# Optimization experiments

Measured on AMD Instinct MI355X. Metric: run time of the kernel, lower is better.

Reference implementation:

```python
import jax, jax.numpy as jnp
import numpy as np

K = 3          # kernel size
KF = K * K     # kernel field = 9
PAD = 1
STRIDE = 1


def _conv(x, w, b):
    y = jax.lax.conv_general_dilated(
        x, w, (STRIDE, STRIDE), [(PAD, PAD), (PAD, PAD)],
        dimension_numbers=('NCHW', 'OIHW', 'NCHW'))
    return y + b[None, :, None, None]


def _bilinear_gather(x, py, px):
    # x: [B,C,H,W]; py/px: [B,KF,Ho,Wo] float sampling coords (zero-pad outside)
    B, C, H, W = x.shape
    xf = x.reshape(B, C, H * W)
    y0 = jnp.floor(py)
    x0 = jnp.floor(px)

    def corner(yc, xc):
        wy = 1.0 - jnp.abs(py - yc)
        wx = 1.0 - jnp.abs(px - xc)
        valid = (yc >= 0) & (yc <= H - 1) & (xc >= 0) & (xc <= W - 1)
        yi = jnp.clip(yc, 0, H - 1).astype(jnp.int32)
        xi = jnp.clip(xc, 0, W - 1).astype(jnp.int32)
        idx = (yi * W + xi).reshape(B, -1)               # [B, KF*Ho*Wo]
        v = jax.vmap(lambda f, i: f[:, i])(xf, idx)      # [B, C, KF*Ho*Wo]
        wgt = (wy * wx * valid.astype(x.dtype)).reshape(B, 1, -1)
        return v * wgt

    return (corner(y0, x0) + corner(y0, x0 + 1) +
            corner(y0 + 1, x0) + corner(y0 + 1, x0 + 1))  # [B,C,KF*Ho*Wo]


def _deform_conv(x, offset, mask, w, b):
    # modulated deformable conv v2 (mmcv offset layout: [y,x] interleaved per kernel pt)
    B, C, H, W = x.shape
    Ho, Wo = mask.shape[2], mask.shape[3]
    kh, kw = jnp.meshgrid(jnp.arange(K), jnp.arange(K), indexing='ij')
    kh = kh.reshape(-1).astype(x.dtype)   # [KF]
    kw = kw.reshape(-1).astype(x.dtype)
    base_y = (jnp.arange(Ho) * STRIDE - PAD).astype(x.dtype)
    base_x = (jnp.arange(Wo) * STRIDE - PAD).astype(x.dtype)
    off = offset.reshape(B, KF, 2, Ho, Wo)
    py = base_y[None, None, :, None] + kh[None, :, None, None] + off[:, :, 0]
    px = base_x[None, None, None, :] + kw[None, :, None, None] + off[:, :, 1]
    val = _bilinear_gather(x, py, px).reshape(B, C, KF, Ho, Wo)
    val = val * mask[:, None]                             # modulate
    out = jnp.einsum('bckhw,ock->bohw', val, w.reshape(w.shape[0], C, KF))
    return out + b[None, :, None, None]


def setup_inputs() -> dict:
    key = jax.random.key(0)
    k1, k2, k3 = jax.random.split(key, 3)
    B, C, H, W = 8, 64, 128, 128
    x = jax.random.normal(k1, (B, C, H, W), dtype=jnp.float32)
    w_om = jax.random.normal(k2, (3 * KF, C, K, K), dtype=jnp.float32) * 0.02
    b_om = jnp.zeros((3 * KF,), dtype=jnp.float32)
    w_dc = jax.random.normal(k3, (64, C, K, K), dtype=jnp.float32) * 0.05
    b_dc = jnp.zeros((64,), dtype=jnp.float32)
    return {"x": x, "w_om": w_om, "b_om": b_om, "w_dc": w_dc, "b_dc": b_dc}


def reference(x, w_om, b_om, w_dc, b_dc):
    om = _conv(x, w_om, b_om)                 # [B, 3*KF, H, W]
    offset = om[:, :2 * KF]
    mask = 2.0 * jax.nn.sigmoid(om[:, 2 * KF:])
    return _deform_conv(x, offset, mask, w_dc, b_dc)
```

## Files before the change

### kernel.cpp

```cpp
#include <hip/hip_runtime.h>
#include <cmath>

#define IH 128
#define IW 128
#define NB 8

typedef __attribute__((ext_vector_type(8))) short bf16x8;
typedef __attribute__((ext_vector_type(4))) float f32x4;

union U4B8 { uint4 u; bf16x8 h; };

#define OFFM_OFF 0
#define XT_OFF   3538944
#define WTDC_OFF (3538944 + 4194304)
#define WTOM_OFF (3538944 + 4194304 + 18432)

__device__ __forceinline__ unsigned short f32_to_bf16(float f) {
    unsigned int u = __float_as_uint(f);
    u += 0x7fffu + ((u >> 16) & 1u);
    return (unsigned short)(u >> 16);
}

__global__ void transpose_weights(const float* __restrict__ w_dc,
                                  const float* __restrict__ w_om,
                                  unsigned short* __restrict__ wt_dc16,
                                  unsigned short* __restrict__ wt_om16) {
    int idx = blockIdx.x * blockDim.x + threadIdx.x;
    if (idx < 9 * 64 * 64) {
        int k = idx >> 12;
        int o = (idx >> 6) & 63;
        int c = idx & 63;
        wt_dc16[idx] = f32_to_bf16(w_dc[(o * 64 + c) * 9 + k]);
    }
    if (idx < 9 * 32 * 64) {
        int k = idx >> 11;
        int o = (idx >> 6) & 31;
        int c = idx & 63;
        wt_om16[idx] = (o < 27) ? f32_to_bf16(w_om[(o * 64 + c) * 9 + k])
                                : (unsigned short)0;
    }
}

__global__ __launch_bounds__(256) void transpose_x(
        const float* __restrict__ x, unsigned short* __restrict__ xT) {
    __shared__ float t[64 * 65];
    const int tid = threadIdx.x;
    const int blk = blockIdx.x;
    const int b = blk >> 8;
    const int rem = blk & 255;
    const int h = rem >> 1;
    const int w0 = (rem & 1) << 6;

    for (int i = tid; i < 4096; i += 256) {
        const int c = i >> 6;
        const int w = i & 63;
        t[w * 65 + c] = x[(((size_t)(b * 64 + c)) << 14) + (h << 7) + w0 + w];
    }
    __syncthreads();
    const int c2 = (tid & 31) * 2;
    ushort2* dst = (ushort2*)(xT + (((size_t)b << 20)) + ((size_t)((h << 7) + w0)) * 64 + c2);
#pragma unroll
    for (int p = 0; p < 8; ++p) {
        const int w = (tid >> 5) + p * 8;
        ushort2 u;
        u.x = f32_to_bf16(t[w * 65 + c2]);
        u.y = f32_to_bf16(t[w * 65 + c2 + 1]);
        dst[(size_t)w * 32] = u;
    }
}

__global__ __launch_bounds__(256) void conv_om_mfma(
        const unsigned short* __restrict__ xT,
        const float* __restrict__ b_om,
        const unsigned short* __restrict__ wt_om16,
        float* __restrict__ offm) {
    __shared__ __align__(16) unsigned short win[198 * 72];
    __shared__ __align__(16) unsigned short wks[2][32 * 72];

    const int tid = threadIdx.x;
    const int bid = blockIdx.x;
    const int swz = ((bid & 7) << 8) + (bid >> 3);
    const int b = swz >> 8;
    const int rem = swz & 255;
    const int h = rem >> 1;
    const int w0 = (rem & 1) << 6;
    const int wid = tid >> 6;
    const int lane = tid & 63;
    const int ln15 = lane & 15;
    const int quad = lane >> 4;

    for (int idx = tid; idx < 1584; idx += 256) {
        const int pos = idx >> 3;
        const int part = idx & 7;
        const int r = pos / 66;
        const int xx = pos - r * 66;
        const int y = h + r - 1;
        const int xg = w0 + xx - 1;
        uint4 v = make_uint4(0u, 0u, 0u, 0u);
        if (y >= 0 && y < IH && xg >= 0 && xg < IW)
            v = *(const uint4*)(xT + (((size_t)b << 20) + (((y << 7) + xg) << 6) + (part << 3)));
        *(uint4*)&win[pos * 72 + part * 8] = v;
    }
    {
        const int o = tid >> 3;
        const int part = tid & 7;
        *(uint4*)&wks[0][o * 72 + part * 8] =
            *(const uint4*)(wt_om16 + (o << 6) + (part << 3));
    }
    __syncthreads();

    f32x4 acc[2] = {{0.f, 0.f, 0.f, 0.f}, {0.f, 0.f, 0.f, 0.f}};

    for (int k = 0; k < 9; ++k) {
        const int buf = k & 1;
        if (k < 8) {
            const int o = tid >> 3;
            const int part = tid & 7;
            *(uint4*)&wks[buf ^ 1][o * 72 + part * 8] =
                *(const uint4*)(wt_om16 + ((k + 1) << 11) + (o << 6) + (part << 3));
        }
        const int kh = k / 3;
        const int kw = k - kh * 3;
        const int posb = kh * 66 + wid * 16 + ln15 + kw;
        const unsigned short* wb = wks[buf];
#pragma unroll
        for (int ch = 0; ch < 2; ++ch) {
            const int c = (ch << 5) + (quad << 3);
            U4B8 a, b0, b1;
            a.u  = *(const uint4*)&win[posb * 72 + c];
            b0.u = *(const uint4*)&wb[ln15 * 72 + c];
            b1.u = *(const uint4*)&wb[(16 + ln15) * 72 + c];
            acc[0] = __builtin_amdgcn_mfma_f32_16x16x32_bf16(a.h, b0.h, acc[0], 0, 0, 0);
            acc[1] = __builtin_amdgcn_mfma_f32_16x16x32_bf16(a.h, b1.h, acc[1], 0, 0, 0);
        }
        __syncthreads();
    }

    const int px0 = wid * 16 + quad * 4;
#pragma unroll
    for (int ot = 0; ot < 2; ++ot) {
        const int o = (ot << 4) + ln15;
        if (o >= 27) continue;
        const float bias = b_om[o];
        float4 r;
        r.x = acc[ot][0] + bias;
        r.y = acc[ot][1] + bias;
        r.z = acc[ot][2] + bias;
        r.w = acc[ot][3] + bias;
        if (o >= 18) {
            r.x = 2.0f / (1.0f + __expf(-r.x));
            r.y = 2.0f / (1.0f + __expf(-r.y));
            r.z = 2.0f / (1.0f + __expf(-r.z));
            r.w = 2.0f / (1.0f + __expf(-r.w));
        }
        *(float4*)&offm[(((size_t)(b * 27 + o)) << 14) + (h << 7) + w0 + px0] = r;
    }
}

__device__ __forceinline__ void corner2(const unsigned short* __restrict__ p,
                                        float wgt, float* v) {
    const uint4 a = *(const uint4*)p;
    const uint4 c = *(const uint4*)(p + 32);
    unsigned int u[8] = {a.x, a.y, a.z, a.w, c.x, c.y, c.z, c.w};
#pragma unroll
    for (int i = 0; i < 8; ++i) {
        v[2 * i]     += wgt * __uint_as_float(u[i] << 16);
        v[2 * i + 1] += wgt * __uint_as_float(u[i] & 0xffff0000u);
    }
}

__device__ __forceinline__ void gather_frags(
        const unsigned short* __restrict__ xb, const float* __restrict__ offs,
        int k, int lpx, int h, int w0, int quad, U4B8& a0, U4B8& a1) {
    const float offy = offs[(k << 1) * 64 + lpx];
    const float offx = offs[((k << 1) + 1) * 64 + lpx];
    const float msk  = offs[(18 + k) * 64 + lpx];
    const int kh = k / 3;
    const int kw = k - kh * 3;
    const float py  = (float)(h + kh - 1) + offy;
    const float pxf = (float)(w0 + lpx + kw - 1) + offx;
    const float y0f = floorf(py);
    const float x0f = floorf(pxf);
    const float fy = py - y0f;
    const float fx = pxf - x0f;
    const float wy0 = 1.0f - fy, wx0 = 1.0f - fx;
    const float vy0 = (y0f >= 0.0f && y0f <= 127.0f) ? 1.0f : 0.0f;
    const float vy1 = (y0f >= -1.0f && y0f <= 126.0f) ? 1.0f : 0.0f;
    const float vx0 = (x0f >= 0.0f && x0f <= 127.0f) ? 1.0f : 0.0f;
    const float vx1 = (x0f >= -1.0f && x0f <= 126.0f) ? 1.0f : 0.0f;
    const float w00 = wy0 * wx0 * vy0 * vx0;
    const float w01 = wy0 * fx  * vy0 * vx1;
    const float w10 = fy  * wx0 * vy1 * vx0;
    const float w11 = fy  * fx  * vy1 * vx1;
    const int y0i = min(max((int)y0f, 0), 127);
    const int y1i = min(max((int)y0f + 1, 0), 127);
    const int x0i = min(max((int)x0f, 0), 127);
    const int x1i = min(max((int)x0f + 1, 0), 127);

    float v[16];
#pragma unroll
    for (int i = 0; i < 16; ++i) v[i] = 0.0f;
    const int cofs = quad << 3;
    corner2(xb + ((((size_t)((y0i << 7) + x0i)) << 6) + cofs), w00, v);
    corner2(xb + ((((size_t)((y0i << 7) + x1i)) << 6) + cofs), w01, v);
    corner2(xb + ((((size_t)((y1i << 7) + x0i)) << 6) + cofs), w10, v);
    corner2(xb + ((((size_t)((y1i << 7) + x1i)) << 6) + cofs), w11, v);

    unsigned int pk[8];
#pragma unroll
    for (int i = 0; i < 8; ++i) {
        const unsigned int lo = f32_to_bf16(v[2 * i] * msk);
        const unsigned int hi = f32_to_bf16(v[2 * i + 1] * msk);
        pk[i] = lo | (hi << 16);
    }
    a0.u = make_uint4(pk[0], pk[1], pk[2], pk[3]);
    a1.u = make_uint4(pk[4], pk[5], pk[6], pk[7]);
}

__global__ __launch_bounds__(256) void deform_mfma(
        const unsigned short* __restrict__ xT,
        const float* __restrict__ b_dc,
        const float* __restrict__ offm,
        const unsigned short* __restrict__ wt_dc16,
        float* __restrict__ out) {
    __shared__ __align__(16) float offs[27 * 64];
    __shared__ __align__(16) unsigned short wks[2][64 * 72];

    const int tid = threadIdx.x;
    const int bid = blockIdx.x;
    const int swz = ((bid & 7) << 8) + (bid >> 3);
    const int b = swz >> 8;
    const int rem = swz & 255;
    const int h = rem >> 1;
    const int w0 = (rem & 1) << 6;
    const int wid = tid >> 6;
    const int lane = tid & 63;
    const int ln15 = lane & 15;
    const int quad = lane >> 4;
    const int lpx = (wid << 4) + ln15;

    for (int i = tid; i < 1728; i += 256) {
        const int ch = i >> 6;
        const int px = i & 63;
        offs[i] = offm[(((size_t)(b * 27 + ch)) << 14) + (h << 7) + w0 + px];
    }
    for (int s = tid; s < 512; s += 256) {
        const int o = s >> 3;
        const int part = s & 7;
        *(uint4*)&wks[0][o * 72 + part * 8] =
            *(const uint4*)(wt_dc16 + (o << 6) + (part << 3));
    }
    __syncthreads();

    const unsigned short* xb = xT + ((size_t)b << 20);

    f32x4 acc[4];
#pragma unroll
    for (int i = 0; i < 4; ++i) acc[i] = (f32x4){0.f, 0.f, 0.f, 0.f};

    U4B8 a0c, a1c;
    gather_frags(xb, offs, 0, lpx, h, w0, quad, a0c, a1c);

    for (int k = 0; k < 9; ++k) {
        const int buf = k & 1;
        U4B8 a0n, a1n;
        a0n.u = make_uint4(0u, 0u, 0u, 0u);
        a1n.u = make_uint4(0u, 0u, 0u, 0u);
        if (k < 8) {
            for (int s = tid; s < 512; s += 256) {
                const int o = s >> 3;
                const int part = s & 7;
                *(uint4*)&wks[buf ^ 1][o * 72 + part * 8] =
                    *(const uint4*)(wt_dc16 + ((k + 1) << 12) + (o << 6) + (part << 3));
            }
            gather_frags(xb, offs, k + 1, lpx, h, w0, quad, a0n, a1n);
        }
        const unsigned short* wb = wks[buf];
#pragma unroll
        for (int ot = 0; ot < 4; ++ot) {
            U4B8 b0, b1;
            const unsigned short* base = &wb[((ot << 4) + ln15) * 72 + (quad << 3)];
            b0.u = *(const uint4*)base;
            b1.u = *(const uint4*)(base + 32);
            acc[ot] = __builtin_amdgcn_mfma_f32_16x16x32_bf16(a0c.h, b0.h, acc[ot], 0, 0, 0);
            acc[ot] = __builtin_amdgcn_mfma_f32_16x16x32_bf16(a1c.h, b1.h, acc[ot], 0, 0, 0);
        }
        __syncthreads();
        a0c = a0n;
        a1c = a1n;
    }

#pragma unroll
    for (int ot = 0; ot < 4; ++ot) {
        const int o = (ot << 4) + ln15;
        const float bias = b_dc[o];
        float4 r;
        r.x = acc[ot][0] + bias;
        r.y = acc[ot][1] + bias;
        r.z = acc[ot][2] + bias;
        r.w = acc[ot][3] + bias;
        *(float4*)&out[(((size_t)(b * 64 + o)) << 14) + (h << 7) + w0 + (wid << 4) + (quad << 2)] = r;
    }
}

extern "C" void kernel_launch(void* const* d_in, const int* in_sizes, int n_in,
                              void* d_out, int out_size, void* d_ws, size_t ws_size,
                              hipStream_t stream) {
    const float* x    = (const float*)d_in[0];
    const float* w_om = (const float*)d_in[1];
    const float* b_om = (const float*)d_in[2];
    const float* w_dc = (const float*)d_in[3];
    const float* b_dc = (const float*)d_in[4];
    float* out = (float*)d_out;
    float* ws  = (float*)d_ws;

    float* offm = ws + OFFM_OFF;
    unsigned short* xT      = (unsigned short*)(ws + XT_OFF);
    unsigned short* wt_dc16 = (unsigned short*)(ws + WTDC_OFF);
    unsigned short* wt_om16 = (unsigned short*)(ws + WTOM_OFF);

    const int n_blocks = NB * IH * (IW / 64);

    transpose_weights<<<144, 256, 0, stream>>>(w_dc, w_om, wt_dc16, wt_om16);
    transpose_x<<<NB * IH * 2, 256, 0, stream>>>(x, xT);
    conv_om_mfma<<<n_blocks, 256, 0, stream>>>(xT, b_om, wt_om16, offm);
    deform_mfma<<<n_blocks, 256, 0, stream>>>(xT, b_dc, offm, wt_dc16, out);
}
```

Baseline: 182.8 us.

## Split bilinear gather into async issue and deferred packed-FMA combine

The deformable gather is split in two. Raw corner loads for the next kernel point are issued a full iteration ahead and held in registers, and the bilinear combine runs just before the MFMAs. The combine now uses v_pk_fma_f32 with the mask folded into the corner weights, plus v_cvt_pk_bf16_f32 for packing. The weight tile prefetch goes through registers, the k-loop is fully unrolled, and the trailing barrier is replaced with a raw s_barrier after an lgkmcnt wait. This aims to hide gather latency behind the MFMA work and cut VALU instructions, at the cost of more registers (16 uint4 live) and a lighter synchronisation that depends on the manual waitcnt being correct.

Result: faster. 177.6 us (-2.9%).

```diff
diff --git a/kernel.cpp b/kernel.cpp
--- a/kernel.cpp
+++ b/kernel.cpp
@@ -7,6 +7,7 @@
 
 typedef __attribute__((ext_vector_type(8))) short bf16x8;
 typedef __attribute__((ext_vector_type(4))) float f32x4;
+typedef __attribute__((ext_vector_type(2))) float f32x2;
 
 union U4B8 { uint4 u; bf16x8 h; };
 
@@ -157,21 +158,9 @@
     }
 }
 
-__device__ __forceinline__ void corner2(const unsigned short* __restrict__ p,
-                                        float wgt, float* v) {
-    const uint4 a = *(const uint4*)p;
-    const uint4 c = *(const uint4*)(p + 32);
-    unsigned int u[8] = {a.x, a.y, a.z, a.w, c.x, c.y, c.z, c.w};
-#pragma unroll
-    for (int i = 0; i < 8; ++i) {
-        v[2 * i]     += wgt * __uint_as_float(u[i] << 16);
-        v[2 * i + 1] += wgt * __uint_as_float(u[i] & 0xffff0000u);
-    }
-}
-
-__device__ __forceinline__ void gather_frags(
+__device__ __forceinline__ void issue_gather(
         const unsigned short* __restrict__ xb, const float* __restrict__ offs,
-        int k, int lpx, int h, int w0, int quad, U4B8& a0, U4B8& a1) {
+        int k, int lpx, int h, int w0, int quad, uint4* g, float* cw) {
     const float offy = offs[(k << 1) * 64 + lpx];
     const float offx = offs[((k << 1) + 1) * 64 + lpx];
     const float msk  = offs[(18 + k) * 64 + lpx];
@@ -188,31 +177,51 @@
     const float vy1 = (y0f >= -1.0f && y0f <= 126.0f) ? 1.0f : 0.0f;
     const float vx0 = (x0f >= 0.0f && x0f <= 127.0f) ? 1.0f : 0.0f;
     const float vx1 = (x0f >= -1.0f && x0f <= 126.0f) ? 1.0f : 0.0f;
-    const float w00 = wy0 * wx0 * vy0 * vx0;
-    const float w01 = wy0 * fx  * vy0 * vx1;
-    const float w10 = fy  * wx0 * vy1 * vx0;
-    const float w11 = fy  * fx  * vy1 * vx1;
+    cw[0] = wy0 * wx0 * vy0 * vx0 * msk;
+    cw[1] = wy0 * fx  * vy0 * vx1 * msk;
+    cw[2] = fy  * wx0 * vy1 * vx0 * msk;
+    cw[3] = fy  * fx  * vy1 * vx1 * msk;
     const int y0i = min(max((int)y0f, 0), 127);
     const int y1i = min(max((int)y0f + 1, 0), 127);
     const int x0i = min(max((int)x0f, 0), 127);
     const int x1i = min(max((int)x0f + 1, 0), 127);
-
-    float v[16];
-#pragma unroll
-    for (int i = 0; i < 16; ++i) v[i] = 0.0f;
     const int cofs = quad << 3;
-    corner2(xb + ((((size_t)((y0i << 7) + x0i)) << 6) + cofs), w00, v);
-    corner2(xb + ((((size_t)((y0i << 7) + x1i)) << 6) + cofs), w01, v);
-    corner2(xb + ((((size_t)((y1i << 7) + x0i)) << 6) + cofs), w10, v);
-    corner2(xb + ((((size_t)((y1i << 7) + x1i)) << 6) + cofs), w11, v);
-
+    const unsigned short* p00 = xb + ((((size_t)((y0i << 7) + x0i)) << 6) + cofs);
+    const unsigned short* p01 = xb + ((((size_t)((y0i << 7) + x1i)) << 6) + cofs);
+    const unsigned short* p10 = xb + ((((size_t)((y1i << 7) + x0i)) << 6) + cofs);
+    const unsigned short* p11 = xb + ((((size_t)((y1i << 7) + x1i)) << 6) + cofs);
+    g[0] = *(const uint4*)p00;  g[1] = *(const uint4*)(p00 + 32);
+    g[2] = *(const uint4*)p01;  g[3] = *(const uint4*)(p01 + 32);
+    g[4] = *(const uint4*)p10;  g[5] = *(const uint4*)(p10 + 32);
+    g[6] = *(const uint4*)p11;  g[7] = *(const uint4*)(p11 + 32);
+}
+
+__device__ __forceinline__ void pack_frags(const uint4* g, const float* cw,
+                                           U4B8& a0, U4B8& a1) {
+    f32x2 v2[8];
+#pragma unroll
+    for (int i = 0; i < 8; ++i) v2[i] = (f32x2){0.f, 0.f};
+#pragma unroll
+    for (int c = 0; c < 4; ++c) {
+        f32x2 w2;
+        w2.x = cw[c];
+        w2.y = cw[c];
+        const uint4 ga = g[2 * c];
+        const uint4 gb = g[2 * c + 1];
+        const unsigned int u[8] = {ga.x, ga.y, ga.z, ga.w, gb.x, gb.y, gb.z, gb.w};
+#pragma unroll
+        for (int i = 0; i < 8; ++i) {
+            f32x2 x2;
+            x2.x = __uint_as_float(u[i] << 16);
+            x2.y = __uint_as_float(u[i] & 0xffff0000u);
+            asm("v_pk_fma_f32 %0, %1, %2, %0" : "+v"(v2[i]) : "v"(x2), "v"(w2));
+        }
+    }
     unsigned int pk[8];
 #pragma unroll
-    for (int i = 0; i < 8; ++i) {
-        const unsigned int lo = f32_to_bf16(v[2 * i] * msk);
-        const unsigned int hi = f32_to_bf16(v[2 * i + 1] * msk);
-        pk[i] = lo | (hi << 16);
-    }
+    for (int i = 0; i < 8; ++i)
+        asm("v_cvt_pk_bf16_f32 %0, %1, %2"
+            : "=v"(pk[i]) : "v"(v2[i].x), "v"(v2[i].y));
     a0.u = make_uint4(pk[0], pk[1], pk[2], pk[3]);
     a1.u = make_uint4(pk[4], pk[5], pk[6], pk[7]);
 }
@@ -239,17 +248,14 @@
     const int quad = lane >> 4;
     const int lpx = (wid << 4) + ln15;
 
+    const int so0 = tid >> 3, sp0 = tid & 7;
+    const int so1 = (tid + 256) >> 3, sp1 = tid & 7;
+
     for (int i = tid; i < 1728; i += 256) {
-        const int ch = i >> 6;
-        const int px = i & 63;
-        offs[i] = offm[(((size_t)(b * 27 + ch)) << 14) + (h << 7) + w0 + px];
-    }
-    for (int s = tid; s < 512; s += 256) {
-        const int o = s >> 3;
-        const int part = s & 7;
-        *(uint4*)&wks[0][o * 72 + part * 8] =
-            *(const uint4*)(wt_dc16 + (o << 6) + (part << 3));
-    }
+        offs[i] = offm[(((size_t)(b * 27 + (i >> 6))) << 14) + (h << 7) + w0 + (i & 63)];
+    }
+    *(uint4*)&wks[0][so0 * 72 + sp0 * 8] = *(const uint4*)(wt_dc16 + (so0 << 6) + (sp0 << 3));
+    *(uint4*)&wks[0][so1 * 72 + sp1 * 8] = *(const uint4*)(wt_dc16 + (so1 << 6) + (sp1 << 3));
     __syncthreads();
 
     const unsigned short* xb = xT + ((size_t)b << 20);
@@ -258,36 +264,38 @@
 #pragma unroll
     for (int i = 0; i < 4; ++i) acc[i] = (f32x4){0.f, 0.f, 0.f, 0.f};
 
-    U4B8 a0c, a1c;
-    gather_frags(xb, offs, 0, lpx, h, w0, quad, a0c, a1c);
-
+    uint4 g[2][8];
+    float cw[2][4];
+    issue_gather(xb, offs, 0, lpx, h, w0, quad, g[0], cw[0]);
+
+#pragma unroll
     for (int k = 0; k < 9; ++k) {
-        const int buf = k & 1;
-        U4B8 a0n, a1n;
-        a0n.u = make_uint4(0u, 0u, 0u, 0u);
-        a1n.u = make_uint4(0u, 0u, 0u, 0u);
+        const int cur = k & 1;
+        const int nxt = cur ^ 1;
         if (k < 8) {
-            for (int s = tid; s < 512; s += 256) {
-                const int o = s >> 3;
-                const int part = s & 7;
-                *(uint4*)&wks[buf ^ 1][o * 72 + part * 8] =
-                    *(const uint4*)(wt_dc16 + ((k + 1) << 12) + (o << 6) + (part << 3));
-            }
-            gather_frags(xb, offs, k + 1, lpx, h, w0, quad, a0n, a1n);
-        }
-        const unsigned short* wb = wks[buf];
+            const uint4 wv0 = *(const uint4*)(wt_dc16 + ((k + 1) << 12) + (so0 << 6) + (sp0 << 3));
+            const uint4 wv1 = *(const uint4*)(wt_dc16 + ((k + 1) << 12) + (so1 << 6) + (sp1 << 3));
+            issue_gather(xb, offs, k + 1, lpx, h, w0, quad, g[nxt], cw[nxt]);
+            *(uint4*)&wks[nxt][so0 * 72 + sp0 * 8] = wv0;
+            *(uint4*)&wks[nxt][so1 * 72 + sp1 * 8] = wv1;
+        }
+        U4B8 a0, a1;
+        pack_frags(g[cur], cw[cur], a0, a1);
+        const unsigned short* wb = wks[cur];
 #pragma unroll
         for (int ot = 0; ot < 4; ++ot) {
             U4B8 b0, b1;
             const unsigned short* base = &wb[((ot << 4) + ln15) * 72 + (quad << 3)];
             b0.u = *(const uint4*)base;
             b1.u = *(const uint4*)(base + 32);
-            acc[ot] = __builtin_amdgcn_mfma_f32_16x16x32_bf16(a0c.h, b0.h, acc[ot], 0, 0, 0);
-            acc[ot] = __builtin_amdgcn_mfma_f32_16x16x32_bf16(a1c.h, b1.h, acc[ot], 0, 0, 0);
-        }
-        __syncthreads();
-        a0c = a0n;
-        a1c = a1n;
+            acc[ot] = __builtin_amdgcn_mfma_f32_16x16x32_bf16(a0.h, b0.h, acc[ot], 0, 0, 0);
+            acc[ot] = __builtin_amdgcn_mfma_f32_16x16x32_bf16(a1.h, b1.h, acc[ot], 0, 0, 0);
+        }
+        if (k < 8) {
+            asm volatile("s_waitcnt lgkmcnt(0)" ::: "memory");
+            __builtin_amdgcn_s_barrier();
+            __builtin_amdgcn_sched_barrier(0);
+        }
     }
 
 #pragma unroll
```
